# Kernel tuning notes

Hardware: AMD Instinct MI355X
Metric: run time of the kernel (lower is better)

The kernel has to match this reference:

```python
import jax, jax.numpy as jnp
import numpy as np

NUM_HEADS = 12

def setup_inputs() -> dict:
    key = jax.random.key(0)
    ks = jax.random.split(key, 8)
    B, N, C = 8, 1024, 768
    H = NUM_HEADS
    return {
        "x": jax.random.normal(ks[0], (B, N, C), dtype=jnp.float32),
        "relative_position_index": jax.random.randint(ks[1], (N, N), 0, 2048, dtype=jnp.int64),
        "qkv_weight": jax.random.normal(ks[2], (3 * C, C), dtype=jnp.float32) * 0.02,
        "q_bias": jax.random.normal(ks[3], (C,), dtype=jnp.float32) * 0.02,
        "v_bias": jax.random.normal(ks[4], (C,), dtype=jnp.float32) * 0.02,
        "proj_weight": jax.random.normal(ks[5], (C, C), dtype=jnp.float32) * 0.02,
        "proj_bias": jax.random.normal(ks[6], (C,), dtype=jnp.float32) * 0.02,
        "rel_pos_bias_table": jax.random.normal(ks[7], (2048, H), dtype=jnp.float32) * 0.02,
    }

def reference(x, relative_position_index, qkv_weight, q_bias, v_bias, proj_weight, proj_bias, rel_pos_bias_table):
    B, N, C = x.shape
    H = NUM_HEADS
    d = C // H
    scale = d ** (-0.5)
    # qkv bias: (q_bias, zeros, v_bias) as in the torch module
    qkv_b = jnp.concatenate([q_bias, jnp.zeros_like(v_bias), v_bias])
    qkv = x @ qkv_weight.T + qkv_b  # [B,N,3C]
    qkv = qkv.reshape(B, N, 3, H, d).transpose(2, 0, 3, 1, 4)  # [3,B,H,N,d]
    q, k, v = qkv[0], qkv[1], qkv[2]
    attn = jnp.einsum("bhnd,bhmd->bhnm", q * scale, k)  # [B,H,N,N]
    # relative position bias: table lookup [N,N,H] -> [H,N,N]
    bias = rel_pos_bias_table[relative_position_index].transpose(2, 0, 1)
    attn = attn + bias[None]
    attn = jax.nn.softmax(attn, axis=-1)
    out = jnp.einsum("bhnm,bhmd->bhnd", attn, v)  # [B,H,N,d]
    out = out.transpose(0, 2, 1, 3).reshape(B, N, C)
    return out @ proj_weight.T + proj_bias
```

## Files before the change

### kernel.cpp

```cpp
#include <hip/hip_runtime.h>

typedef unsigned short ushort_t;
typedef __bf16 bf16x8 __attribute__((ext_vector_type(8)));
typedef float f32x4 __attribute__((ext_vector_type(4)));
typedef unsigned int u32x4 __attribute__((ext_vector_type(4)));

#define MFMA(a, b, c) __builtin_amdgcn_mfma_f32_16x16x32_bf16((a), (b), (c), 0, 0, 0)

#define BATCH 8
#define SEQ 1024
#define CDIM 768
#define NH 12
#define HD 64
#define MTOT (BATCH * SEQ)
#define THREEC (3 * CDIM)
#define KVB 64
#define LOG2E 1.44269504088896f

__device__ __forceinline__ ushort_t f2bf(float f) {
    unsigned int u = __builtin_bit_cast(unsigned int, f);
    u = (u + 0x7FFFu + ((u >> 16) & 1u)) >> 16;
    return (ushort_t)u;
}
__device__ __forceinline__ float bf2f(ushort_t b) {
    unsigned int u = ((unsigned int)b) << 16;
    return __builtin_bit_cast(float, u);
}
__device__ __forceinline__ ushort_t bfbits(float f) {
    __bf16 h = (__bf16)f;
    return __builtin_bit_cast(ushort_t, h);
}
__device__ __forceinline__ unsigned int pack2bf(float a, float b) {
    ushort2 p;
    p.x = bfbits(a);
    p.y = bfbits(b);
    return __builtin_bit_cast(unsigned int, p);
}

typedef const __attribute__((address_space(1))) unsigned int* gas_ptr;
typedef __attribute__((address_space(3))) unsigned int* las_ptr;

__device__ __forceinline__ void async16(const ushort_t* g, ushort_t* l) {
    __builtin_amdgcn_global_load_lds((gas_ptr)(const void*)g, (las_ptr)(void*)l, 16, 0, 0);
}

#define WAITVM_(N) asm volatile("s_waitcnt vmcnt(" #N ")" ::: "memory")
#define WAITVM(N) WAITVM_(N)
#define SCHEDB __builtin_amdgcn_sched_barrier(0)

__global__ __launch_bounds__(256) void k_convert(const float* __restrict__ x,
                                                 const float* __restrict__ wq,
                                                 const float* __restrict__ wp,
                                                 ushort_t* __restrict__ xb,
                                                 ushort_t* __restrict__ wqb,
                                                 ushort_t* __restrict__ wpb) {
    const int NX = MTOT * CDIM / 4;
    const int NQ = THREEC * CDIM / 4;
    const int NP = CDIM * CDIM / 4;
    int i = blockIdx.x * 256 + threadIdx.x;
    const float4* src;
    ushort_t* dst;
    int off;
    if (i < NX) { src = (const float4*)x; dst = xb; off = i; }
    else if (i < NX + NQ) { src = (const float4*)wq; dst = wqb; off = i - NX; }
    else if (i < NX + NQ + NP) { src = (const float4*)wp; dst = wpb; off = i - NX - NQ; }
    else return;
    float4 v = src[off];
    ushort4 o;
    o.x = f2bf(v.x); o.y = f2bf(v.y); o.z = f2bf(v.z); o.w = f2bf(v.w);
    ((ushort4*)dst)[off] = o;
}

__global__ __launch_bounds__(256) void k_bias(const int* __restrict__ rpi,
                                              const float* __restrict__ table,
                                              ushort_t* __restrict__ biasF) {
    __shared__ int idx_s[16][64];
    int tr = blockIdx.x;
    int tcq = blockIdx.y;
    int t = threadIdx.x;
    {
        int r = t >> 4;
        int c4 = (t & 15) * 4;
        int4 v = *(const int4*)&rpi[(tr * 16 + r) * SEQ + tcq * 64 + c4];
        *(int4*)&idx_s[r][c4] = v;
    }
    __syncthreads();
    int j = t >> 6;
    int lane = t & 63;
    int lq = lane >> 4, l15 = lane & 15;
    int tc = tcq * 4 + j;
    int id[4];
#pragma unroll
    for (int rr = 0; rr < 4; rr++) id[rr] = idx_s[l15][j * 16 + lq * 4 + rr];
#pragma unroll
    for (int h = 0; h < NH; h++) {
        ushort4 o;
        o.x = f2bf(table[id[0] * NH + h] * LOG2E);
        o.y = f2bf(table[id[1] * NH + h] * LOG2E);
        o.z = f2bf(table[id[2] * NH + h] * LOG2E);
        o.w = f2bf(table[id[3] * NH + h] * LOG2E);
        *(ushort4*)&biasF[(((h * 64 + tr) * 64 + tc) * 256 + lane * 4)] = o;
    }
}

template <int MODE>
__global__ __launch_bounds__(256) void k_gemm(const ushort_t* __restrict__ A,
                                              const ushort_t* __restrict__ Bw,
                                              const float* __restrict__ biasq,
                                              const float* __restrict__ biasv,
                                              const float* __restrict__ biasp,
                                              ushort_t* __restrict__ qb,
                                              ushort_t* __restrict__ kb,
                                              ushort_t* __restrict__ vT,
                                              float* __restrict__ outp) {
    __shared__ __attribute__((aligned(16))) ushort_t As[128 * 64];
    __shared__ __attribute__((aligned(16))) ushort_t Bs[128 * 64];
    const int K = CDIM;
    int tid = threadIdx.x, wave = tid >> 6, lane = tid & 63;
    int l15 = lane & 15, lq = lane >> 4;
    int wm = wave >> 1, wn = wave & 1;
    int rowBase = blockIdx.y * 128;
    int colBase = blockIdx.x * 128;
    f32x4 acc[4][4] = {};
    int srow = wave * 8 + (lane >> 3);
    int scol = (((lane & 7) ^ (srow & 7))) * 8;
    int l7 = l15 & 7;
    for (int k0 = 0; k0 < K; k0 += 64) {
#pragma unroll
        for (int is = 0; is < 4; is++) {
            async16(A + (rowBase + is * 32 + srow) * K + k0 + scol,
                    As + is * 2048 + tid * 8);
            async16(Bw + (colBase + is * 32 + srow) * K + k0 + scol,
                    Bs + is * 2048 + tid * 8);
        }
        asm volatile("s_waitcnt vmcnt(0)" ::: "memory");
        __syncthreads();
#pragma unroll
        for (int kk = 0; kk < 64; kk += 32) {
            bf16x8 af[4], bfr[4];
#pragma unroll
            for (int mf = 0; mf < 4; mf++)
                af[mf] = *(const bf16x8*)&As[(wm * 64 + mf * 16 + l15) * 64 +
                                             ((((kk >> 3) + lq) ^ l7) * 8)];
#pragma unroll
            for (int nf = 0; nf < 4; nf++)
                bfr[nf] = *(const bf16x8*)&Bs[(wn * 64 + nf * 16 + l15) * 64 +
                                              ((((kk >> 3) + lq) ^ l7) * 8)];
#pragma unroll
            for (int mf = 0; mf < 4; mf++)
#pragma unroll
                for (int nf = 0; nf < 4; nf++)
                    acc[mf][nf] = MFMA(af[mf], bfr[nf], acc[mf][nf]);
        }
        __syncthreads();
    }
#pragma unroll
    for (int mf = 0; mf < 4; mf++) {
#pragma unroll
        for (int nf = 0; nf < 4; nf++) {
            int jc = colBase + wn * 64 + nf * 16 + l15;
            int mg0 = rowBase + wm * 64 + mf * 16 + (lane >> 4) * 4;
            if (MODE == 0) {
                int which = jc / CDIM;
                int co = jc - which * CDIM;
                int b = mg0 >> 10, tok0 = mg0 & 1023;
                int hh = co >> 6, dd = co & 63;
                int bh = b * NH + hh;
                if (which == 0) {
                    float bq_ = biasq[co];
#pragma unroll
                    for (int r = 0; r < 4; r++)
                        qb[(bh * SEQ + tok0 + r) * HD + dd] =
                            f2bf((acc[mf][nf][r] + bq_) * 0.125f);
                } else if (which == 1) {
#pragma unroll
                    for (int r = 0; r < 4; r++)
                        kb[(bh * SEQ + tok0 + r) * HD + dd] = f2bf(acc[mf][nf][r]);
                } else {
                    float bv = biasv[co];
                    ushort4 pk;
                    pk.x = f2bf(acc[mf][nf][0] + bv);
                    pk.y = f2bf(acc[mf][nf][1] + bv);
                    pk.z = f2bf(acc[mf][nf][2] + bv);
                    pk.w = f2bf(acc[mf][nf][3] + bv);
                    *(ushort4*)&vT[(size_t)(bh * HD + dd) * SEQ + tok0] = pk;
                }
            } else {
                float bp_ = biasp[jc];
#pragma unroll
                for (int r = 0; r < 4; r++)
                    outp[(size_t)(mg0 + r) * CDIM + jc] = acc[mf][nf][r] + bp_;
            }
        }
    }
}

__global__ __launch_bounds__(256, 3) void k_attn(const ushort_t* __restrict__ qb,
                                                 const ushort_t* __restrict__ kb,
                                                 const ushort_t* __restrict__ vT,
                                                 const ushort_t* __restrict__ biasF,
                                                 ushort_t* __restrict__ ctx) {
    __shared__ __attribute__((aligned(16))) ushort_t Ks[2][KVB * 64];
    __shared__ __attribute__((aligned(16))) ushort_t Vs[2][KVB * 64];

    int lin = ((int)blockIdx.x & 7) * 96 + ((int)blockIdx.x >> 3);
    int h = lin >> 6;
    int b = (lin >> 3) & 7;
    int qt = lin & 7;
    int bh = b * NH + h;
    int tid = threadIdx.x, w = tid >> 6, lane = tid & 63;
    int l15 = lane & 15, lq = lane >> 4, lq4 = lq * 4;
    int row0 = qt * 128 + w * 32;
    int qtile0 = row0 >> 4;

    const ushort_t* qp = qb + bh * SEQ * HD;
    const ushort_t* kp = kb + bh * SEQ * HD;
    const ushort_t* vp = vT + bh * HD * SEQ;
    const ushort_t* bfp0 = biasF + (size_t)(h * 64 + qtile0) * 64 * 256;
    const ushort_t* bfp1 = bfp0 + 64 * 256;

    int lamA = l15 + 32 * (lq & 1);
    int lamB = lamA + 16;

    int rk0, sk0, rk1, sk1;
    {
        int cid0 = tid;
        rk0 = cid0 >> 3; sk0 = ((cid0 & 7) ^ (rk0 & 7)) * 8;
        int cid1 = 256 + tid;
        rk1 = cid1 >> 3; sk1 = ((cid1 & 7) ^ (rk1 & 7)) * 8;
    }

#define STAGE_K(BUF, C0)                                                    \
    do {                                                                    \
        async16(kp + ((C0) + rk0) * HD + sk0, &Ks[BUF][tid * 8]);           \
        async16(kp + ((C0) + rk1) * HD + sk1, &Ks[BUF][(256 + tid) * 8]);   \
    } while (0)
#define STAGE_V(BUF, C0)                                                    \
    do {                                                                    \
        async16(vp + rk0 * SEQ + (C0) + sk0, &Vs[BUF][tid * 8]);            \
        async16(vp + rk1 * SEQ + (C0) + sk1, &Vs[BUF][(256 + tid) * 8]);    \
    } while (0)

    STAGE_K(0, 0); STAGE_V(0, 0); STAGE_K(1, KVB); STAGE_V(1, KVB);

    bf16x8 qfr00 = *(const bf16x8*)&qp[(row0 + l15) * HD + 8 * lq];
    bf16x8 qfr01 = *(const bf16x8*)&qp[(row0 + l15) * HD + 32 + 8 * lq];
    bf16x8 qfr10 = *(const bf16x8*)&qp[(row0 + 16 + l15) * HD + 8 * lq];
    bf16x8 qfr11 = *(const bf16x8*)&qp[(row0 + 16 + l15) * HD + 32 + 8 * lq];

    f32x4 Oa0[4] = {}, Oa1[4] = {};
    float mi0 = -1e30f, mi1 = -1e30f, li0 = 0.0f, li1 = 0.0f;
    f32x4 accA0[4], accA1[4], accB0[4], accB1[4];
    unsigned int u0[4][2], u1[4][2];

#define QK_BLOCK(AN0, AN1, KN)                                                 \
    do {                                                                       \
        __builtin_amdgcn_s_setprio(1);                                         \
        _Pragma("unroll") for (int n = 0; n < 4; n++) {                        \
            int krow = n * 16 + l15;                                           \
            bf16x8 kf0 = *(const bf16x8*)&(KN)[krow * 64 + ((lq ^ (krow & 7)) * 8)]; \
            bf16x8 kf1 = *(const bf16x8*)&(KN)[krow * 64 + (((lq + 4) ^ (krow & 7)) * 8)]; \
            f32x4 z0 = {};                                                     \
            z0 = MFMA(kf0, qfr00, z0); z0 = MFMA(kf1, qfr01, z0);              \
            (AN0)[n] = z0;                                                     \
            f32x4 z1 = {};                                                     \
            z1 = MFMA(kf0, qfr10, z1); z1 = MFMA(kf1, qfr11, z1);              \
            (AN1)[n] = z1;                                                     \
        }                                                                      \
        __builtin_amdgcn_s_setprio(0);                                         \
    } while (0)

#define SOFTMAX_HALF(ACC, BFR, MI, LI, OA, UH)                                 \
    do {                                                                       \
        f32x4 z[4];                                                            \
        _Pragma("unroll") for (int n = 0; n < 4; n++) {                        \
            z[n][0] = fmaf((ACC)[n][0], LOG2E, bf2f((BFR)[n].x));              \
            z[n][1] = fmaf((ACC)[n][1], LOG2E, bf2f((BFR)[n].y));              \
            z[n][2] = fmaf((ACC)[n][2], LOG2E, bf2f((BFR)[n].z));              \
            z[n][3] = fmaf((ACC)[n][3], LOG2E, bf2f((BFR)[n].w));              \
        }                                                                      \
        float tm;                                                              \
        {                                                                      \
            f32x4 mv;                                                          \
            _Pragma("unroll") for (int j = 0; j < 4; j++)                      \
                mv[j] = fmaxf(fmaxf(z[0][j], z[1][j]), fmaxf(z[2][j], z[3][j])); \
            tm = fmaxf(fmaxf(mv[0], mv[1]), fmaxf(mv[2], mv[3]));              \
        }                                                                      \
        tm = fmaxf(tm, __shfl_xor(tm, 16));                                    \
        tm = fmaxf(tm, __shfl_xor(tm, 32));                                    \
        if (!__all(tm <= (MI) + 8.0f)) {                                       \
            float mn = fmaxf((MI), tm);                                        \
            float al = exp2f((MI) - mn);                                       \
            (MI) = mn; (LI) *= al;                                             \
            _Pragma("unroll") for (int r = 0; r < 4; r++) {                    \
                float alr = __shfl(al, (lane & 48) | (lq4 + r));               \
                (OA)[0][r] *= alr; (OA)[1][r] *= alr;                          \
                (OA)[2][r] *= alr; (OA)[3][r] *= alr;                          \
            }                                                                  \
        }                                                                      \
        f32x4 sv = {};                                                         \
        _Pragma("unroll") for (int n = 0; n < 4; n++) {                        \
            z[n][0] = exp2f(z[n][0] - (MI)); z[n][1] = exp2f(z[n][1] - (MI));  \
            z[n][2] = exp2f(z[n][2] - (MI)); z[n][3] = exp2f(z[n][3] - (MI));  \
            sv += z[n];                                                        \
        }                                                                      \
        float s = (sv[0] + sv[1]) + (sv[2] + sv[3]);                           \
        s += __shfl_xor(s, 16);                                                \
        s += __shfl_xor(s, 32);                                                \
        (LI) += s;                                                             \
        _Pragma("unroll") for (int n = 0; n < 4; n++) {                        \
            (UH)[n][0] = pack2bf(z[n][0], z[n][1]);                            \
            (UH)[n][1] = pack2bf(z[n][2], z[n][3]);                            \
        }                                                                      \
    } while (0)

#define ASSEMBLE(UH, KS, PF)                                                   \
    do {                                                                       \
        unsigned int a0 = __shfl((int)(UH)[2 * (KS)][0], lamA);                \
        unsigned int b0 = __shfl((int)(UH)[2 * (KS) + 1][0], lamA);            \
        unsigned int a1 = __shfl((int)(UH)[2 * (KS)][1], lamA);                \
        unsigned int b1 = __shfl((int)(UH)[2 * (KS) + 1][1], lamA);            \
        unsigned int a2 = __shfl((int)(UH)[2 * (KS)][0], lamB);                \
        unsigned int b2 = __shfl((int)(UH)[2 * (KS) + 1][0], lamB);            \
        unsigned int a3 = __shfl((int)(UH)[2 * (KS)][1], lamB);                \
        unsigned int b3 = __shfl((int)(UH)[2 * (KS) + 1][1], lamB);            \
        bool hi_ = (lq & 2) != 0;                                              \
        u32x4 qd;                                                              \
        qd[0] = hi_ ? b0 : a0; qd[1] = hi_ ? b1 : a1;                          \
        qd[2] = hi_ ? b2 : a2; qd[3] = hi_ ? b3 : a3;                          \
        (PF) = __builtin_bit_cast(bf16x8, qd);                                 \
    } while (0)

#define PV_BLOCK(VC)                                                           \
    do {                                                                       \
        __builtin_amdgcn_s_setprio(1);                                         \
        _Pragma("unroll") for (int ks = 0; ks < 2; ks++) {                     \
            bf16x8 pfa, pfb;                                                   \
            ASSEMBLE(u0, ks, pfa);                                             \
            ASSEMBLE(u1, ks, pfb);                                             \
            _Pragma("unroll") for (int nc = 0; nc < 4; nc++) {                 \
                int vrow = nc * 16 + l15;                                      \
                bf16x8 vf = *(const bf16x8*)&(VC)[vrow * 64 + (((ks * 4 + lq) ^ (vrow & 7)) * 8)]; \
                Oa0[nc] = MFMA(pfa, vf, Oa0[nc]);                              \
                Oa1[nc] = MFMA(pfb, vf, Oa1[nc]);                              \
            }                                                                  \
        }                                                                      \
        __builtin_amdgcn_s_setprio(0);                                         \
    } while (0)

#define ITER(T, AC0, AC1, AN0, AN1, DO_STAGE, DO_QK)                           \
    do {                                                                       \
        WAITVM(0);                                                             \
        SCHEDB;                                                                \
        __builtin_amdgcn_s_barrier();                                          \
        SCHEDB;                                                                \
        const int t_ = (T);                                                    \
        ushort4 bfr0[4], bfr1[4];                                              \
        {                                                                      \
            int kt0 = t_ * 4;                                                  \
            _Pragma("unroll") for (int n = 0; n < 4; n++) {                    \
                bfr0[n] = *(const ushort4*)&bfp0[(kt0 + n) * 256 + lane * 4];  \
                bfr1[n] = *(const ushort4*)&bfp1[(kt0 + n) * 256 + lane * 4];  \
            }                                                                  \
        }                                                                      \
        if (DO_STAGE) STAGE_K(t_ & 1, (t_ + 2) * KVB);                         \
        if (DO_QK) QK_BLOCK(AN0, AN1, Ks[(t_ + 1) & 1]);                       \
        SOFTMAX_HALF(AC0, bfr0, mi0, li0, Oa0, u0);                            \
        SOFTMAX_HALF(AC1, bfr1, mi1, li1, Oa1, u1);                            \
        PV_BLOCK(Vs[t_ & 1]);                                                  \
        if (DO_STAGE) {                                                        \
            SCHEDB;                                                            \
            __builtin_amdgcn_s_barrier();                                      \
            SCHEDB;                                                            \
            STAGE_V(t_ & 1, (t_ + 2) * KVB);                                   \
        }                                                                      \
    } while (0)

    WAITVM(6);
    SCHEDB;
    __builtin_amdgcn_s_barrier();
    SCHEDB;
    QK_BLOCK(accA0, accA1, Ks[0]);

#pragma unroll 1
    for (int tt = 0; tt < 14; tt += 2) {
        ITER(tt,     accA0, accA1, accB0, accB1, 1, 1);
        ITER(tt + 1, accB0, accB1, accA0, accA1, 1, 1);
    }
    ITER(14, accA0, accA1, accB0, accB1, 0, 1);
    ITER(15, accB0, accB1, accA0, accA1, 0, 0);

    float rli0 = 1.0f / li0, rli1 = 1.0f / li1;
#pragma unroll
    for (int r = 0; r < 4; r++) {
        float rl0 = __shfl(rli0, (lane & 48) | (lq4 + r));
        float rl1 = __shfl(rli1, (lane & 48) | (lq4 + r));
#pragma unroll
        for (int nc = 0; nc < 4; nc++) {
            ctx[(size_t)(b * SEQ + row0 + lq4 + r) * CDIM + h * HD + nc * 16 + l15] =
                bfbits(Oa0[nc][r] * rl0);
            ctx[(size_t)(b * SEQ + row0 + 16 + lq4 + r) * CDIM + h * HD + nc * 16 + l15] =
                bfbits(Oa1[nc][r] * rl1);
        }
    }
#undef ITER
#undef PV_BLOCK
#undef ASSEMBLE
#undef SOFTMAX_HALF
#undef QK_BLOCK
#undef STAGE_V
#undef STAGE_K
}

extern "C" void kernel_launch(void* const* d_in, const int* in_sizes, int n_in,
                              void* d_out, int out_size, void* d_ws, size_t ws_size,
                              hipStream_t stream) {
    const float* x = (const float*)d_in[0];
    const int* rpi = (const int*)d_in[1];
    const float* wqkv = (const float*)d_in[2];
    const float* qbias = (const float*)d_in[3];
    const float* vbias = (const float*)d_in[4];
    const float* wproj = (const float*)d_in[5];
    const float* pbias = (const float*)d_in[6];
    const float* table = (const float*)d_in[7];
    float* out = (float*)d_out;

    char* ws = (char*)d_ws;
    ushort_t* xb    = (ushort_t*)(ws + 0);
    ushort_t* wqb   = (ushort_t*)(ws + 12582912);
    ushort_t* wpb   = (ushort_t*)(ws + 16121856);
    ushort_t* qbuf  = (ushort_t*)(ws + 17301504);
    ushort_t* kbuf  = (ushort_t*)(ws + 29884416);
    ushort_t* vTbuf = (ushort_t*)(ws + 42467328);
    ushort_t* ctx   = (ushort_t*)(ws + 55050240);
    ushort_t* biasF = (ushort_t*)(ws + 67633152);

    k_convert<<<8448, 256, 0, stream>>>(x, wqkv, wproj, xb, wqb, wpb);
    k_bias<<<dim3(64, 16), 256, 0, stream>>>(rpi, table, biasF);
    k_gemm<0><<<dim3(THREEC / 128, MTOT / 128), 256, 0, stream>>>(
        xb, wqb, qbias, vbias, nullptr, qbuf, kbuf, vTbuf, nullptr);
    k_attn<<<768, 256, 0, stream>>>(qbuf, kbuf, vTbuf, biasF, ctx);
    k_gemm<1><<<dim3(CDIM / 128, MTOT / 128), 256, 0, stream>>>(
        ctx, wpb, nullptr, nullptr, pbias, nullptr, nullptr, nullptr, out);
}
```

Before: 178.7 us.

## Halve attention query tile to 64 rows per block and double grid

```diff
diff --git a/kernel.cpp b/kernel.cpp
--- a/kernel.cpp
+++ b/kernel.cpp
@@ -195,7 +195,7 @@
     }
 }
 
-__global__ __launch_bounds__(256, 3) void k_attn(const ushort_t* __restrict__ qb,
+__global__ __launch_bounds__(256, 4) void k_attn(const ushort_t* __restrict__ qb,
                                                  const ushort_t* __restrict__ kb,
                                                  const ushort_t* __restrict__ vT,
                                                  const ushort_t* __restrict__ biasF,
@@ -203,21 +203,20 @@
     __shared__ __attribute__((aligned(16))) ushort_t Ks[2][KVB * 64];
     __shared__ __attribute__((aligned(16))) ushort_t Vs[2][KVB * 64];
 
-    int lin = ((int)blockIdx.x & 7) * 96 + ((int)blockIdx.x >> 3);
-    int h = lin >> 6;
-    int b = (lin >> 3) & 7;
-    int qt = lin & 7;
+    int lin = ((int)blockIdx.x & 7) * 192 + ((int)blockIdx.x >> 3);
+    int h = lin >> 7;
+    int b = (lin >> 4) & 7;
+    int qt = lin & 15;
     int bh = b * NH + h;
     int tid = threadIdx.x, w = tid >> 6, lane = tid & 63;
     int l15 = lane & 15, lq = lane >> 4, lq4 = lq * 4;
-    int row0 = qt * 128 + w * 32;
+    int row0 = qt * 64 + w * 16;
     int qtile0 = row0 >> 4;
 
     const ushort_t* qp = qb + bh * SEQ * HD;
     const ushort_t* kp = kb + bh * SEQ * HD;
     const ushort_t* vp = vT + bh * HD * SEQ;
-    const ushort_t* bfp0 = biasF + (size_t)(h * 64 + qtile0) * 64 * 256;
-    const ushort_t* bfp1 = bfp0 + 64 * 256;
+    const ushort_t* bfp = biasF + (size_t)(h * 64 + qtile0) * 64 * 256;
 
     int lamA = l15 + 32 * (lq & 1);
     int lamB = lamA + 16;
@@ -243,17 +242,15 @@
 
     STAGE_K(0, 0); STAGE_V(0, 0); STAGE_K(1, KVB); STAGE_V(1, KVB);
 
-    bf16x8 qfr00 = *(const bf16x8*)&qp[(row0 + l15) * HD + 8 * lq];
-    bf16x8 qfr01 = *(const bf16x8*)&qp[(row0 + l15) * HD + 32 + 8 * lq];
-    bf16x8 qfr10 = *(const bf16x8*)&qp[(row0 + 16 + l15) * HD + 8 * lq];
-    bf16x8 qfr11 = *(const bf16x8*)&qp[(row0 + 16 + l15) * HD + 32 + 8 * lq];
-
-    f32x4 Oa0[4] = {}, Oa1[4] = {};
-    float mi0 = -1e30f, mi1 = -1e30f, li0 = 0.0f, li1 = 0.0f;
-    f32x4 accA0[4], accA1[4], accB0[4], accB1[4];
-    unsigned int u0[4][2], u1[4][2];
-
-#define QK_BLOCK(AN0, AN1, KN)                                                 \
+    bf16x8 qfr0 = *(const bf16x8*)&qp[(row0 + l15) * HD + 8 * lq];
+    bf16x8 qfr1 = *(const bf16x8*)&qp[(row0 + l15) * HD + 32 + 8 * lq];
+
+    f32x4 Oa[4] = {};
+    float mi = -1e30f, li = 0.0f;
+    f32x4 accA[4], accB[4];
+    unsigned int u0[4][2];
+
+#define QK_BLOCK(AN, KN)                                                       \
     do {                                                                       \
         __builtin_amdgcn_s_setprio(1);                                         \
         _Pragma("unroll") for (int n = 0; n < 4; n++) {                        \
@@ -261,16 +258,13 @@
             bf16x8 kf0 = *(const bf16x8*)&(KN)[krow * 64 + ((lq ^ (krow & 7)) * 8)]; \
             bf16x8 kf1 = *(const bf16x8*)&(KN)[krow * 64 + (((lq + 4) ^ (krow & 7)) * 8)]; \
             f32x4 z0 = {};                                                     \
-            z0 = MFMA(kf0, qfr00, z0); z0 = MFMA(kf1, qfr01, z0);              \
-            (AN0)[n] = z0;                                                     \
-            f32x4 z1 = {};                                                     \
-            z1 = MFMA(kf0, qfr10, z1); z1 = MFMA(kf1, qfr11, z1);              \
-            (AN1)[n] = z1;                                                     \
+            z0 = MFMA(kf0, qfr0, z0); z0 = MFMA(kf1, qfr1, z0);                \
+            (AN)[n] = z0;                                                      \
         }                                                                      \
         __builtin_amdgcn_s_setprio(0);                                         \
     } while (0)
 
-#define SOFTMAX_HALF(ACC, BFR, MI, LI, OA, UH)                                 \
+#define SOFTMAX_STEP(ACC, BFR)                                                 \
     do {                                                                       \
         f32x4 z[4];                                                            \
         _Pragma("unroll") for (int n = 0; n < 4; n++) {                        \
@@ -288,42 +282,42 @@
         }                                                                      \
         tm = fmaxf(tm, __shfl_xor(tm, 16));                                    \
         tm = fmaxf(tm, __shfl_xor(tm, 32));                                    \
-        if (!__all(tm <= (MI) + 8.0f)) {                                       \
-            float mn = fmaxf((MI), tm);                                        \
-            float al = exp2f((MI) - mn);                                       \
-            (MI) = mn; (LI) *= al;                                             \
+        if (!__all(tm <= mi + 8.0f)) {                                         \
+            float mn = fmaxf(mi, tm);                                          \
+            float al = exp2f(mi - mn);                                         \
+            mi = mn; li *= al;                                                 \
             _Pragma("unroll") for (int r = 0; r < 4; r++) {                    \
                 float alr = __shfl(al, (lane & 48) | (lq4 + r));               \
-                (OA)[0][r] *= alr; (OA)[1][r] *= alr;                          \
-                (OA)[2][r] *= alr; (OA)[3][r] *= alr;                          \
+                Oa[0][r] *= alr; Oa[1][r] *= alr;                              \
+                Oa[2][r] *= alr; Oa[3][r] *= alr;                              \
             }                                                                  \
         }                                                                      \
         f32x4 sv = {};                                                         \
         _Pragma("unroll") for (int n = 0; n < 4; n++) {                        \
-            z[n][0] = exp2f(z[n][0] - (MI)); z[n][1] = exp2f(z[n][1] - (MI));  \
-            z[n][2] = exp2f(z[n][2] - (MI)); z[n][3] = exp2f(z[n][3] - (MI));  \
+            z[n][0] = exp2f(z[n][0] - mi); z[n][1] = exp2f(z[n][1] - mi);      \
+            z[n][2] = exp2f(z[n][2] - mi); z[n][3] = exp2f(z[n][3] - mi);      \
             sv += z[n];                                                        \
         }                                                                      \
         float s = (sv[0] + sv[1]) + (sv[2] + sv[3]);                           \
         s += __shfl_xor(s, 16);                                                \
         s += __shfl_xor(s, 32);                                                \
-        (LI) += s;                                                             \
+        li += s;                                                               \
         _Pragma("unroll") for (int n = 0; n < 4; n++) {                        \
-            (UH)[n][0] = pack2bf(z[n][0], z[n][1]);                            \
-            (UH)[n][1] = pack2bf(z[n][2], z[n][3]);                            \
-        }                                                                      \
-    } while (0)
-
-#define ASSEMBLE(UH, KS, PF)                                                   \
+            u0[n][0] = pack2bf(z[n][0], z[n][1]);                              \
+            u0[n][1] = pack2bf(z[n][2], z[n][3]);                              \
+        }                                                                      \
+    } while (0)
+
+#define ASSEMBLE(KS, PF)                                                       \
     do {                                                                       \
-        unsigned int a0 = __shfl((int)(UH)[2 * (KS)][0], lamA);                \
-        unsigned int b0 = __shfl((int)(UH)[2 * (KS) + 1][0], lamA);            \
-        unsigned int a1 = __shfl((int)(UH)[2 * (KS)][1], lamA);                \
-        unsigned int b1 = __shfl((int)(UH)[2 * (KS) + 1][1], lamA);            \
-        unsigned int a2 = __shfl((int)(UH)[2 * (KS)][0], lamB);                \
-        unsigned int b2 = __shfl((int)(UH)[2 * (KS) + 1][0], lamB);            \
-        unsigned int a3 = __shfl((int)(UH)[2 * (KS)][1], lamB);                \
-        unsigned int b3 = __shfl((int)(UH)[2 * (KS) + 1][1], lamB);            \
+        unsigned int a0 = __shfl((int)u0[2 * (KS)][0], lamA);                  \
+        unsigned int b0 = __shfl((int)u0[2 * (KS) + 1][0], lamA);              \
+        unsigned int a1 = __shfl((int)u0[2 * (KS)][1], lamA);                  \
+        unsigned int b1 = __shfl((int)u0[2 * (KS) + 1][1], lamA);              \
+        unsigned int a2 = __shfl((int)u0[2 * (KS)][0], lamB);                  \
+        unsigned int b2 = __shfl((int)u0[2 * (KS) + 1][0], lamB);              \
+        unsigned int a3 = __shfl((int)u0[2 * (KS)][1], lamB);                  \
+        unsigned int b3 = __shfl((int)u0[2 * (KS) + 1][1], lamB);              \
         bool hi_ = (lq & 2) != 0;                                              \
         u32x4 qd;                                                              \
         qd[0] = hi_ ? b0 : a0; qd[1] = hi_ ? b1 : a1;                          \
@@ -335,38 +329,33 @@
     do {                                                                       \
         __builtin_amdgcn_s_setprio(1);                                         \
         _Pragma("unroll") for (int ks = 0; ks < 2; ks++) {                     \
-            bf16x8 pfa, pfb;                                                   \
-            ASSEMBLE(u0, ks, pfa);                                             \
-            ASSEMBLE(u1, ks, pfb);                                             \
+            bf16x8 pfa;                                                        \
+            ASSEMBLE(ks, pfa);                                                 \
             _Pragma("unroll") for (int nc = 0; nc < 4; nc++) {                 \
                 int vrow = nc * 16 + l15;                                      \
                 bf16x8 vf = *(const bf16x8*)&(VC)[vrow * 64 + (((ks * 4 + lq) ^ (vrow & 7)) * 8)]; \
-                Oa0[nc] = MFMA(pfa, vf, Oa0[nc]);                              \
-                Oa1[nc] = MFMA(pfb, vf, Oa1[nc]);                              \
+                Oa[nc] = MFMA(pfa, vf, Oa[nc]);                                \
             }                                                                  \
         }                                                                      \
         __builtin_amdgcn_s_setprio(0);                                         \
     } while (0)
 
-#define ITER(T, AC0, AC1, AN0, AN1, DO_STAGE, DO_QK)                           \
+#define ITER(T, AC, AN, DO_STAGE, DO_QK)                                       \
     do {                                                                       \
         WAITVM(0);                                                             \
         SCHEDB;                                                                \
         __builtin_amdgcn_s_barrier();                                          \
         SCHEDB;                                                                \
         const int t_ = (T);                                                    \
-        ushort4 bfr0[4], bfr1[4];                                              \
+        ushort4 bfr0[4];                                                       \
         {                                                                      \
             int kt0 = t_ * 4;                                                  \
-            _Pragma("unroll") for (int n = 0; n < 4; n++) {                    \
-                bfr0[n] = *(const ushort4*)&bfp0[(kt0 + n) * 256 + lane * 4];  \
-                bfr1[n] = *(const ushort4*)&bfp1[(kt0 + n) * 256 + lane * 4];  \
-            }                                                                  \
+            _Pragma("unroll") for (int n = 0; n < 4; n++)                      \
+                bfr0[n] = *(const ushort4*)&bfp[(kt0 + n) * 256 + lane * 4];   \
         }                                                                      \
         if (DO_STAGE) STAGE_K(t_ & 1, (t_ + 2) * KVB);                         \
-        if (DO_QK) QK_BLOCK(AN0, AN1, Ks[(t_ + 1) & 1]);                       \
-        SOFTMAX_HALF(AC0, bfr0, mi0, li0, Oa0, u0);                            \
-        SOFTMAX_HALF(AC1, bfr1, mi1, li1, Oa1, u1);                            \
+        if (DO_QK) QK_BLOCK(AN, Ks[(t_ + 1) & 1]);                             \
+        SOFTMAX_STEP(AC, bfr0);                                                \
         PV_BLOCK(Vs[t_ & 1]);                                                  \
         if (DO_STAGE) {                                                        \
             SCHEDB;                                                            \
@@ -380,33 +369,30 @@
     SCHEDB;
     __builtin_amdgcn_s_barrier();
     SCHEDB;
-    QK_BLOCK(accA0, accA1, Ks[0]);
+    QK_BLOCK(accA, Ks[0]);
 
 #pragma unroll 1
     for (int tt = 0; tt < 14; tt += 2) {
-        ITER(tt,     accA0, accA1, accB0, accB1, 1, 1);
-        ITER(tt + 1, accB0, accB1, accA0, accA1, 1, 1);
-    }
-    ITER(14, accA0, accA1, accB0, accB1, 0, 1);
-    ITER(15, accB0, accB1, accA0, accA1, 0, 0);
-
-    float rli0 = 1.0f / li0, rli1 = 1.0f / li1;
+        ITER(tt,     accA, accB, 1, 1);
+        ITER(tt + 1, accB, accA, 1, 1);
+    }
+    ITER(14, accA, accB, 0, 1);
+    ITER(15, accB, accA, 0, 0);
+
+    float rli = 1.0f / li;
 #pragma unroll
     for (int r = 0; r < 4; r++) {
-        float rl0 = __shfl(rli0, (lane & 48) | (lq4 + r));
-        float rl1 = __shfl(rli1, (lane & 48) | (lq4 + r));
+        float rl = __shfl(rli, (lane & 48) | (lq4 + r));
 #pragma unroll
         for (int nc = 0; nc < 4; nc++) {
             ctx[(size_t)(b * SEQ + row0 + lq4 + r) * CDIM + h * HD + nc * 16 + l15] =
-                bfbits(Oa0[nc][r] * rl0);
-            ctx[(size_t)(b * SEQ + row0 + 16 + lq4 + r) * CDIM + h * HD + nc * 16 + l15] =
-                bfbits(Oa1[nc][r] * rl1);
+                bfbits(Oa[nc][r] * rl);
         }
     }
 #undef ITER
 #undef PV_BLOCK
 #undef ASSEMBLE
-#undef SOFTMAX_HALF
+#undef SOFTMAX_STEP
 #undef QK_BLOCK
 #undef STAGE_V
 #undef STAGE_K
@@ -439,7 +425,7 @@
     k_bias<<<dim3(64, 16), 256, 0, stream>>>(rpi, table, biasF);
     k_gemm<0><<<dim3(THREEC / 128, MTOT / 128), 256, 0, stream>>>(
         xb, wqb, qbias, vbias, nullptr, qbuf, kbuf, vTbuf, nullptr);
-    k_attn<<<768, 256, 0, stream>>>(qbuf, kbuf, vTbuf, biasF, ctx);
+    k_attn<<<1536, 256, 0, stream>>>(qbuf, kbuf, vTbuf, biasF, ctx);
     k_gemm<1><<<dim3(CDIM / 128, MTOT / 128), 256, 0, stream>>>(
         ctx, wpb, nullptr, nullptr, pbias, nullptr, nullptr, nullptr, out);
 }
```

New measurement: 170.3 us. 4.7% less time.
